# Kernel optimization log

Measured on AMD Instinct MI355X. Metric: run time of the kernel, lower is better.

## Reference

```python
import jax, jax.numpy as jnp
import numpy as np
from jax import lax

DN = ('NCHW', 'OIHW', 'NCHW')
BETA = 0.25


def _conv(x, w, b, stride, pad):
    y = lax.conv_general_dilated(x, w, (stride, stride), [(pad, pad), (pad, pad)],
                                 dimension_numbers=DN)
    return y + b[None, :, None, None]


def _convT(x, w, b, stride, pad, opad):
    # torch ConvTranspose2d(w: [in,out,kh,kw]) == dilated conv with flipped, transposed kernel
    k = w.shape[2]
    wf = jnp.transpose(w, (1, 0, 2, 3))[:, :, ::-1, ::-1]
    lo = k - 1 - pad
    hi = k - 1 - pad + opad
    y = lax.conv_general_dilated(x, wf, (1, 1), [(lo, hi), (lo, hi)],
                                 lhs_dilation=(stride, stride), dimension_numbers=DN)
    return y + b[None, :, None, None]


def setup_inputs() -> dict:
    key = jax.random.key(0)
    ks = jax.random.split(key, 16)
    s = 0.05
    inp = {
        'x': jax.random.normal(ks[0], (64, 3, 125, 125), jnp.float32),
        'enc_w1': jax.random.normal(ks[1], (32, 3, 3, 3), jnp.float32) * s,
        'enc_b1': jnp.zeros((32,), jnp.float32),
        'enc_w2': jax.random.normal(ks[2], (64, 32, 3, 3), jnp.float32) * s,
        'enc_b2': jnp.zeros((64,), jnp.float32),
        'enc_w3': jax.random.normal(ks[3], (64, 64, 1, 1), jnp.float32) * s,
        'enc_b3': jnp.zeros((64,), jnp.float32),
        'codebook': jax.random.normal(ks[4], (512, 64), jnp.float32),
        'dec_w1': jax.random.normal(ks[5], (64, 64, 3, 3), jnp.float32) * s,  # torch [in,out,kh,kw]
        'dec_b1': jnp.zeros((64,), jnp.float32),
        'dec_w2': jax.random.normal(ks[6], (64, 32, 3, 3), jnp.float32) * s,
        'dec_b2': jnp.zeros((32,), jnp.float32),
        'dec_w3': jax.random.normal(ks[7], (32, 3, 2, 2), jnp.float32) * s,
        'dec_b3': jnp.zeros((3,), jnp.float32),
    }
    return inp


def reference(x, enc_w1, enc_b1, enc_w2, enc_b2, enc_w3, enc_b3, codebook,
              dec_w1, dec_b1, dec_w2, dec_b2, dec_w3, dec_b3):
    # Encoder
    z = jax.nn.relu(_conv(x, enc_w1, enc_b1, 2, 1))
    z = jax.nn.relu(_conv(z, enc_w2, enc_b2, 2, 1))
    z = _conv(z, enc_w3, enc_b3, 1, 0)  # [B, D, h, w]

    # VQ (training mode)
    zp = jnp.transpose(z, (0, 2, 3, 1))  # [B, h, w, D]
    flat = zp.reshape(-1, zp.shape[-1])  # [N, D]
    d = (jnp.sum(flat * flat, axis=1, keepdims=True)
         + jnp.sum(codebook * codebook, axis=1)
         - 2.0 * flat @ codebook.T)  # [N, K]
    idx = jnp.argmin(d, axis=1)
    q = codebook[idx].reshape(zp.shape)

    q_latent_loss = jnp.mean((q - lax.stop_gradient(zp)) ** 2)
    e_latent_loss = jnp.mean((zp - lax.stop_gradient(q)) ** 2)
    e_q_loss = q_latent_loss + BETA * e_latent_loss

    q_st = zp + lax.stop_gradient(q - zp)  # straight-through
    e = jnp.transpose(q_st, (0, 3, 1, 2))

    # Decoder
    h = jax.nn.relu(_convT(e, dec_w1, dec_b1, 2, 1, 1))
    h = jax.nn.relu(_convT(h, dec_w2, dec_b2, 2, 1, 1))
    x_recon = _convT(h, dec_w3, dec_b3, 1, 2, 0)

    recon_loss = jnp.sum((x_recon - x) ** 2)
    loss_sum = e_q_loss + recon_loss
    return (loss_sum, e_q_loss, recon_loss, x_recon)
```

## Files before the change

kernel.cpp:

```cpp
#include <hip/hip_runtime.h>

#define DEV __device__ __forceinline__
typedef unsigned short u16;
typedef __bf16 bf16x8 __attribute__((ext_vector_type(8)));
typedef float f32x4 __attribute__((ext_vector_type(4)));

DEV u16 f2bf(float f) {
  unsigned u = __float_as_uint(f);
  u += 0x7FFF + ((u >> 16) & 1);
  return (u16)(u >> 16);
}


__global__ __launch_bounds__(256) void k_prep(
    const float* __restrict__ ew1, const float* __restrict__ ew2,
    const float* __restrict__ ew3, const float* __restrict__ dw1,
    const float* __restrict__ dw2, const float* __restrict__ dw3,
    const float* __restrict__ cb,
    float* __restrict__ wc1p, float* __restrict__ wc3p,
    u16* __restrict__ w3f, float* __restrict__ c2,
    u16* __restrict__ w2f, u16* __restrict__ wt1f, u16* __restrict__ wt2f,
    u16* __restrict__ cbf,
    const float* __restrict__ x, float* __restrict__ xp) {
  if (blockIdx.x >= 582) {
    int idx = (blockIdx.x - 582) * 256 + threadIdx.x;
    int c4 = idx & 31;
    int r  = (idx >> 5) % 129;
    int cbp = (idx >> 5) / 129;
    int ih = r - 1;
    float4 v = make_float4(0.f, 0.f, 0.f, 0.f);
    if ((unsigned)ih < 125u) {
      const float* rp = x + (cbp * 125 + ih) * 125;
      int iw0 = c4 * 4 - 1;
      if (iw0 >= 0)        v.x = rp[iw0];
      if (iw0 + 1 < 125)   v.y = rp[iw0 + 1];
      if (iw0 + 2 < 125)   v.z = rp[iw0 + 2];
      if (iw0 + 3 < 125)   v.w = rp[iw0 + 3];
    }
    *(float4*)(xp + (cbp * 129 + r) * 128 + c4 * 4) = v;
    return;
  }
  int i = blockIdx.x * 256 + threadIdx.x;
  if (i < 864) {
    int cl = i & 7; int t = i >> 3; int tap = t % 9; t /= 9; int ci = t % 3; int cog = t / 3;
    wc1p[i] = ew1[((cog * 8 + cl) * 3 + ci) * 9 + tap];
  } else if (i < 4960) {
    int j = i - 864; int cl = j & 7; int t = j >> 3; int ci = t & 63; int cog = t >> 6;
    wc3p[j] = ew3[(cog * 8 + cl) * 64 + ci];
  } else if (i < 9056) {
    int j = i - 4960;
    int jj = j & 7; int lane = (j >> 3) & 63; int tp = (j >> 9) & 3; int hl = j >> 11;
    int kh = tp >> 1, kw = tp & 1;
    int ci = ((lane >> 4) << 3) + jj; int co = lane & 15;
    float wv = (co < 3) ? dw3[((ci * 3 + co) * 2 + kh) * 2 + kw] : 0.f;
    u16 hi = f2bf(wv);
    if (hl == 0) w3f[j] = hi;
    else         w3f[j] = f2bf(wv - __uint_as_float((unsigned)hi << 16));
  } else if (i < 9568) {
    int k = i - 9056;
    const float4* c4 = (const float4*)(cb + (k << 6));
    float s = 0.f;
    #pragma unroll
    for (int q = 0; q < 16; ++q) { float4 v = c4[q]; s += v.x*v.x + v.y*v.y + v.z*v.z + v.w*v.w; }
    c2[k] = s;
  } else if (i < 28000) {
    int j = i - 9568;
    int jj = j & 7; int lane = (j >> 3) & 63; int nf = (j >> 9) & 3; int kt = j >> 11;
    int kh = kt / 3, kw = kt % 3;
    int ci = ((lane >> 4) << 3) + jj; int co = (nf << 4) + (lane & 15);
    w2f[j] = f2bf(ew2[((co * 32 + ci) * 3 + kh) * 3 + kw]);
  } else if (i < 64864) {
    int j = i - 28000;
    int jj = j & 7; int lane = (j >> 3) & 63; int nf = (j >> 9) & 3; int s = (j >> 11) & 1; int kt = j >> 12;
    int kh = kt / 3, kw = kt % 3;
    int ci = (s << 5) + ((lane >> 4) << 3) + jj; int co = (nf << 4) + (lane & 15);
    wt1f[j] = f2bf(dw1[((ci * 64 + co) * 3 + kh) * 3 + kw]);
  } else if (i < 83296) {
    int j = i - 64864;
    int jj = j & 7; int lane = (j >> 3) & 63; int nf = (j >> 9) & 1; int s = (j >> 10) & 1; int kt = j >> 11;
    int kh = kt / 3, kw = kt % 3;
    int ci = (s << 5) + ((lane >> 4) << 3) + jj; int co = (nf << 4) + (lane & 15);
    wt2f[j] = f2bf(dw2[((ci * 32 + co) * 3 + kh) * 3 + kw]);
  } else if (i < 148832) {
    int j = i - 83296;
    int jj = j & 7; int lane = (j >> 3) & 63; int nt = (j >> 9) & 31; int ks = (j >> 14) & 1; int hl = j >> 15;
    int ci = (ks << 5) + ((lane >> 4) << 3) + jj;
    int code = (nt << 4) + (lane & 15);
    float v = cb[(code << 6) + ci];
    u16 hi = f2bf(v);
    cbf[j] = hl ? f2bf(v - __uint_as_float((unsigned)hi << 16)) : hi;
  }
}

__global__ __launch_bounds__(256) void k_conv1(
    const float* __restrict__ xp, const float* __restrict__ wp,
    const float* __restrict__ bias, u16* __restrict__ z1t) {
  __shared__ u16 st[256 * 34];
  int t = threadIdx.x;
  int slab = blockIdx.x & 15, b = blockIdx.x >> 4;
  int tx = t & 15, ty = (t >> 4) & 3, cg = t >> 6;
  int oh = slab * 4 + ty;
  int co0 = cg * 8;
  const float* wcg = wp + cg * 216;
  float acc[8][4];
  #pragma unroll
  for (int c = 0; c < 8; ++c) {
    float bv = bias[co0 + c];
    #pragma unroll
    for (int s = 0; s < 4; ++s) acc[c][s] = bv;
  }
  #pragma unroll
  for (int ci = 0; ci < 3; ++ci) {
    #pragma unroll
    for (int kh = 0; kh < 3; ++kh) {
      const float* rp = xp + ((b * 3 + ci) * 129 + (2 * oh + kh)) * 128 + 8 * tx;
      float4 qa = *(const float4*)rp;
      float4 qb = *(const float4*)(rp + 4);
      float v8 = rp[8];
      float v[9] = {qa.x, qa.y, qa.z, qa.w, qb.x, qb.y, qb.z, qb.w, v8};
      #pragma unroll
      for (int kw = 0; kw < 3; ++kw) {
        const float* wq = wcg + (ci * 9 + kh * 3 + kw) * 8;
        float4 wa = *(const float4*)wq;
        float4 wb = *(const float4*)(wq + 4);
        float w8[8] = {wa.x, wa.y, wa.z, wa.w, wb.x, wb.y, wb.z, wb.w};
        #pragma unroll
        for (int s = 0; s < 4; ++s) {
          float in = v[2 * s + kw];
          #pragma unroll
          for (int c = 0; c < 8; ++c) acc[c][s] = fmaf(in, w8[c], acc[c][s]);
        }
      }
    }
  }
  #pragma unroll
  for (int s = 0; s < 4; ++s) {
    bool wok = (tx * 4 + s) < 63;
    unsigned p0 = 0, p1 = 0, p2 = 0, p3 = 0;
    if (wok) {
      p0 = f2bf(fmaxf(acc[0][s], 0.f)) | ((unsigned)f2bf(fmaxf(acc[1][s], 0.f)) << 16);
      p1 = f2bf(fmaxf(acc[2][s], 0.f)) | ((unsigned)f2bf(fmaxf(acc[3][s], 0.f)) << 16);
      p2 = f2bf(fmaxf(acc[4][s], 0.f)) | ((unsigned)f2bf(fmaxf(acc[5][s], 0.f)) << 16);
      p3 = f2bf(fmaxf(acc[6][s], 0.f)) | ((unsigned)f2bf(fmaxf(acc[7][s], 0.f)) << 16);
    }
    int lpix = tx * 16 + ty * 4 + s;
    *(uint4*)&st[lpix * 34 + co0] = make_uint4(p0, p1, p2, p3);
  }
  __syncthreads();
  {
    int p = t;
    int ow = (p >> 4) * 4 + (p & 3);
    int ohl = (p >> 2) & 3;
    int oho = slab * 4 + ohl;
    if (oho < 63) {
      const u16* lp = &st[p * 34];
      uint4 a0 = *(const uint4*)(lp);
      uint4 a1 = *(const uint4*)(lp + 8);
      uint4 a2 = *(const uint4*)(lp + 16);
      uint4 a3 = *(const uint4*)(lp + 24);
      uint4* gp = (uint4*)(z1t + ((b * 63 + oho) * 64 + ow) * 32);
      gp[0] = a0; gp[1] = a1; gp[2] = a2; gp[3] = a3;
    }
  }
}

__global__ __launch_bounds__(256) void k_conv2(
    const u16* __restrict__ z1t, const u16* __restrict__ wf,
    const float* __restrict__ bias, float* __restrict__ z2) {
  int t = threadIdx.x;
  int lane = t & 63, wv = t >> 6;
  int n = lane & 15, q = lane >> 4;
  int raw = blockIdx.x;
  int wg = ((raw & 7) << 8) + (raw >> 3);
  int oh = wg & 31, b = wg >> 5;
  int xt = wv & 1, ch = wv >> 1;
  int xA = xt * 16 + n;
  f32x4 acc[2] = {{0,0,0,0},{0,0,0,0}};
  #pragma unroll
  for (int kh = 0; kh < 3; ++kh) {
    int ih = 2 * oh - 1 + kh;
    bool yok = (unsigned)ih < 63u;
    #pragma unroll
    for (int kw = 0; kw < 3; ++kw) {
      int iw = 2 * xA - 1 + kw;
      bool ok = yok && (iw >= 0);
      bf16x8 a = {};
      if (ok) a = *(const bf16x8*)(z1t + ((b * 63 + ih) * 64 + iw) * 32 + q * 8);
      int kt = kh * 3 + kw;
      const u16* wb = wf + ((kt << 2) + (ch << 1)) * 512 + lane * 8;
      bf16x8 b0 = *(const bf16x8*)wb;
      bf16x8 b1 = *(const bf16x8*)(wb + 512);
      acc[0] = __builtin_amdgcn_mfma_f32_16x16x32_bf16(a, b0, acc[0], 0, 0, 0);
      acc[1] = __builtin_amdgcn_mfma_f32_16x16x32_bf16(a, b1, acc[1], 0, 0, 0);
    }
  }
  #pragma unroll
  for (int j = 0; j < 2; ++j) {
    int co = ((ch << 1) + j) * 16 + n;
    float bv = bias[co];
    float4 rv = make_float4(fmaxf(acc[j][0] + bv, 0.f), fmaxf(acc[j][1] + bv, 0.f),
                            fmaxf(acc[j][2] + bv, 0.f), fmaxf(acc[j][3] + bv, 0.f));
    *(float4*)(z2 + ((b * 64 + co) * 32 + oh) * 32 + xt * 16 + q * 4) = rv;
  }
}

__global__ __launch_bounds__(256) void k_conv3(
    const float* __restrict__ in, const float* __restrict__ wp,
    const float* __restrict__ bias, float* __restrict__ z3,
    u16* __restrict__ z3h, u16* __restrict__ z3l) {
  __shared__ u16 lh[128 * 72];
  __shared__ u16 ll[128 * 72];
  int t = threadIdx.x;
  int pxg = blockIdx.x & 7; int b = blockIdx.x >> 3;
  int pxi = t & 31, cog = t >> 5;
  int px0 = pxg * 128 + pxi * 4;
  const float* wcg = wp + cog * 512;
  int co0 = cog * 8;
  float acc[8][4];
  #pragma unroll
  for (int c = 0; c < 8; ++c) {
    float bv = bias[co0 + c];
    #pragma unroll
    for (int s = 0; s < 4; ++s) acc[c][s] = bv;
  }
  const float* ip = in + (b << 16) + px0;
  for (int ci = 0; ci < 64; ++ci) {
    float4 v = *(const float4*)(ip + (ci << 10));
    float4 wa = *(const float4*)(wcg + ci * 8);
    float4 wb = *(const float4*)(wcg + ci * 8 + 4);
    float w8[8] = {wa.x, wa.y, wa.z, wa.w, wb.x, wb.y, wb.z, wb.w};
    #pragma unroll
    for (int c = 0; c < 8; ++c) {
      acc[c][0] = fmaf(v.x, w8[c], acc[c][0]);
      acc[c][1] = fmaf(v.y, w8[c], acc[c][1]);
      acc[c][2] = fmaf(v.z, w8[c], acc[c][2]);
      acc[c][3] = fmaf(v.w, w8[c], acc[c][3]);
    }
  }
  float* op = z3 + ((b << 6) + co0) * 1024 + px0;
  #pragma unroll
  for (int c = 0; c < 8; ++c)
    *(float4*)(op + (c << 10)) = make_float4(acc[c][0], acc[c][1], acc[c][2], acc[c][3]);
  #pragma unroll
  for (int s = 0; s < 4; ++s) {
    unsigned h[4], l[4];
    #pragma unroll
    for (int g = 0; g < 4; ++g) {
      float v0 = acc[2 * g][s], v1 = acc[2 * g + 1][s];
      u16 h0 = f2bf(v0), h1 = f2bf(v1);
      u16 l0 = f2bf(v0 - __uint_as_float((unsigned)h0 << 16));
      u16 l1 = f2bf(v1 - __uint_as_float((unsigned)h1 << 16));
      h[g] = h0 | ((unsigned)h1 << 16);
      l[g] = l0 | ((unsigned)l1 << 16);
    }
    int la = (pxi * 4 + s) * 72 + co0;
    *(uint4*)&lh[la] = make_uint4(h[0], h[1], h[2], h[3]);
    *(uint4*)&ll[la] = make_uint4(l[0], l[1], l[2], l[3]);
  }
  __syncthreads();
  {
    int p = t >> 1, half = t & 1;
    int la = p * 72 + half * 32;
    uint4 h0 = *(uint4*)&lh[la],      h1 = *(uint4*)&lh[la + 8];
    uint4 h2 = *(uint4*)&lh[la + 16], h3 = *(uint4*)&lh[la + 24];
    uint4 l0 = *(uint4*)&ll[la],      l1 = *(uint4*)&ll[la + 8];
    uint4 l2 = *(uint4*)&ll[la + 16], l3 = *(uint4*)&ll[la + 24];
    long gp = ((long)b * 1024 + pxg * 128 + p) * 64 + half * 32;
    uint4* oh = (uint4*)(z3h + gp);
    uint4* ol = (uint4*)(z3l + gp);
    oh[0] = h0; oh[1] = h1; oh[2] = h2; oh[3] = h3;
    ol[0] = l0; ol[1] = l1; ol[2] = l2; ol[3] = l3;
  }
}

__global__ __launch_bounds__(256) void k_vqpf(
    const u16* __restrict__ z3h, const u16* __restrict__ z3l,
    const u16* __restrict__ cbf, const float* __restrict__ c2v,
    const float* __restrict__ z3, const float* __restrict__ cb,
    u16* __restrict__ et, float* __restrict__ acc) {
  int t = threadIdx.x;
  int lane = t & 63, wv = t >> 6;
  int n = lane & 15, q = lane >> 4;
  int p0 = blockIdx.x * 64;
  bf16x8 Ah[4][2], Al[4][2];
  #pragma unroll
  for (int mt = 0; mt < 4; ++mt) {
    const u16* ap = z3h + (p0 + mt * 16 + n) * 64 + q * 8;
    const u16* al = z3l + (p0 + mt * 16 + n) * 64 + q * 8;
    Ah[mt][0] = *(const bf16x8*)ap;  Ah[mt][1] = *(const bf16x8*)(ap + 32);
    Al[mt][0] = *(const bf16x8*)al;  Al[mt][1] = *(const bf16x8*)(al + 32);
  }
  float bs[4][4]; int bix[4][4];
  #pragma unroll
  for (int mt = 0; mt < 4; ++mt)
    #pragma unroll
    for (int r = 0; r < 4; ++r) { bs[mt][r] = 3.4e38f; bix[mt][r] = 0; }
  for (int nt0 = 0; nt0 < 8; ++nt0) {
    int nt = wv * 8 + nt0;
    const u16* bp = cbf + lane * 8;
    bf16x8 Bh0 = *(const bf16x8*)(bp + (nt << 9));
    bf16x8 Bh1 = *(const bf16x8*)(bp + ((32 + nt) << 9));
    bf16x8 Bl0 = *(const bf16x8*)(bp + ((64 + nt) << 9));
    bf16x8 Bl1 = *(const bf16x8*)(bp + ((96 + nt) << 9));
    float c2 = c2v[(nt << 4) + n];
    #pragma unroll
    for (int mt = 0; mt < 4; ++mt) {
      f32x4 a = {0.f, 0.f, 0.f, 0.f};
      a = __builtin_amdgcn_mfma_f32_16x16x32_bf16(Ah[mt][0], Bh0, a, 0, 0, 0);
      a = __builtin_amdgcn_mfma_f32_16x16x32_bf16(Ah[mt][1], Bh1, a, 0, 0, 0);
      a = __builtin_amdgcn_mfma_f32_16x16x32_bf16(Al[mt][0], Bh0, a, 0, 0, 0);
      a = __builtin_amdgcn_mfma_f32_16x16x32_bf16(Al[mt][1], Bh1, a, 0, 0, 0);
      a = __builtin_amdgcn_mfma_f32_16x16x32_bf16(Ah[mt][0], Bl0, a, 0, 0, 0);
      a = __builtin_amdgcn_mfma_f32_16x16x32_bf16(Ah[mt][1], Bl1, a, 0, 0, 0);
      int idx = (nt << 4) + n;
      #pragma unroll
      for (int r = 0; r < 4; ++r) {
        float sc = fmaf(-2.f, a[r], c2);
        if (sc < bs[mt][r]) { bs[mt][r] = sc; bix[mt][r] = idx; }
      }
    }
  }
  #pragma unroll
  for (int off = 8; off > 0; off >>= 1) {
    #pragma unroll
    for (int mt = 0; mt < 4; ++mt)
      #pragma unroll
      for (int r = 0; r < 4; ++r) {
        float os = __shfl_xor(bs[mt][r], off, 16);
        int oi = __shfl_xor(bix[mt][r], off, 16);
        if (os < bs[mt][r] || (os == bs[mt][r] && oi < bix[mt][r])) {
          bs[mt][r] = os; bix[mt][r] = oi;
        }
      }
  }
  __shared__ float ls[4][64];
  __shared__ int   li[4][64];
  __shared__ int   lfin[64];
  if (n == 0) {
    #pragma unroll
    for (int mt = 0; mt < 4; ++mt)
      #pragma unroll
      for (int r = 0; r < 4; ++r) {
        int px = mt * 16 + q * 4 + r;
        ls[wv][px] = bs[mt][r];
        li[wv][px] = bix[mt][r];
      }
  }
  __syncthreads();
  if (t < 64) {
    float best = ls[0][t]; int bi = li[0][t];
    #pragma unroll
    for (int w = 1; w < 4; ++w) {
      float s = ls[w][t]; int ii = li[w][t];
      if (s < best || (s == best && ii < bi)) { best = s; bi = ii; }
    }
    lfin[t] = bi;
  }
  __syncthreads();
  int pxl = t >> 2, ciq = t & 3;
  int ng = p0 + pxl;
  int bb = ng >> 10, hw = ng & 1023;
  int bi = lfin[pxl];
  const float* zp = z3 + (bb << 16) + hw;
  const float4* cq = (const float4*)(cb + (bi << 6) + (ciq << 4));
  float lsum = 0.f;
  unsigned pk[8];
  #pragma unroll
  for (int i = 0; i < 4; ++i) {
    float4 c = cq[i];
    int cbase = (ciq << 4) + (i << 2);
    float zv, df;
    zv = zp[(cbase + 0) << 10]; df = c.x - zv; lsum = fmaf(df, df, lsum);
    zv = zp[(cbase + 1) << 10]; df = c.y - zv; lsum = fmaf(df, df, lsum);
    zv = zp[(cbase + 2) << 10]; df = c.z - zv; lsum = fmaf(df, df, lsum);
    zv = zp[(cbase + 3) << 10]; df = c.w - zv; lsum = fmaf(df, df, lsum);
    pk[2 * i]     = f2bf(c.x) | ((unsigned)f2bf(c.y) << 16);
    pk[2 * i + 1] = f2bf(c.z) | ((unsigned)f2bf(c.w) << 16);
  }
  uint4* ep = (uint4*)(et + ((long)ng << 6) + (ciq << 4));
  ep[0] = make_uint4(pk[0], pk[1], pk[2], pk[3]);
  ep[1] = make_uint4(pk[4], pk[5], pk[6], pk[7]);
  __shared__ float red[256];
  red[t] = lsum; __syncthreads();
  #pragma unroll
  for (int s = 128; s > 0; s >>= 1) {
    if (t < s) red[t] += red[t + s];
    __syncthreads();
  }
  if (t == 0) atomicAdd(acc + 0, red[0]);
}

__global__ __launch_bounds__(256) void k_convT1(
    const u16* __restrict__ et, const u16* __restrict__ wf,
    const float* __restrict__ bias, u16* __restrict__ h1t) {
  __shared__ u16 wl[36 * 512];
  __shared__ u16 st[4][64 * 34];
  int t = threadIdx.x;
  int lane = t & 63, wv = t >> 6;
  int yw = wv & 1, xt = wv >> 1;
  int raw = blockIdx.x;
  int wg = ((raw & 7) << 7) + (raw >> 3);
  int cog = wg & 1;
  int yg = (wg >> 1) & 7;
  int b = wg >> 4;
  {
    const uint4* gw = (const uint4*)wf;
    uint4* lw = (uint4*)wl;
    #pragma unroll
    for (int k = 0; k < 9; ++k) {
      int i = t + 256 * k;
      int slot = i >> 6, within = i & 63;
      int kt = slot >> 2, j = (slot >> 1) & 1, ks = slot & 1;
      int goff = (kt << 12) + (((ks << 2) + (cog << 1) + j) << 9);
      lw[i] = gw[(goff >> 3) + within];
    }
  }
  int n = lane & 15, q = lane >> 4;
  int m = xt * 16 + n;
  __syncthreads();
  for (int iter = 0; iter < 2; ++iter) {
    int y = yg * 4 + iter * 2 + yw;
    const u16* base0 = et + (((b * 32 + y) * 32) << 6) + q * 8;
    bf16x8 P00a, P00b, P01a = {}, P01b = {}, P10a = {}, P10b = {}, P11a = {}, P11b = {};
    { const u16* p = base0 + (m << 6); P00a = *(const bf16x8*)p; P00b = *(const bf16x8*)(p + 32); }
    if (m + 1 < 32) { const u16* p = base0 + ((m + 1) << 6); P01a = *(const bf16x8*)p; P01b = *(const bf16x8*)(p + 32); }
    if (y + 1 < 32) {
      const u16* base1 = base0 + (32 << 6);
      { const u16* p = base1 + (m << 6); P10a = *(const bf16x8*)p; P10b = *(const bf16x8*)(p + 32); }
      if (m + 1 < 32) { const u16* p = base1 + ((m + 1) << 6); P11a = *(const bf16x8*)p; P11b = *(const bf16x8*)(p + 32); }
    }
    f32x4 accE[2][2] = {};
    f32x4 accO[2][2] = {};
    #pragma unroll
    for (int kw = 0; kw < 3; ++kw) {
      int pwi = (kw == 1) ? 0 : 1;
      bf16x8 A0a = (kw == 0) ? P01a : P00a;
      bf16x8 A0b = (kw == 0) ? P01b : P00b;
      bf16x8 A1a = (kw == 0) ? P11a : P10a;
      bf16x8 A1b = (kw == 0) ? P11b : P10b;
      #pragma unroll
      for (int j = 0; j < 2; ++j) {
        const u16* wE  = wl + ((((3 + kw) << 2) + (j << 1)) << 9) + lane * 8;
        const u16* wO0 = wl + (((kw << 2) + (j << 1)) << 9) + lane * 8;
        const u16* wO2 = wl + ((((6 + kw) << 2) + (j << 1)) << 9) + lane * 8;
        bf16x8 bE0 = *(const bf16x8*)wE;
        bf16x8 bE1 = *(const bf16x8*)(wE + 512);
        accE[j][pwi] = __builtin_amdgcn_mfma_f32_16x16x32_bf16(A0a, bE0, accE[j][pwi], 0, 0, 0);
        accE[j][pwi] = __builtin_amdgcn_mfma_f32_16x16x32_bf16(A0b, bE1, accE[j][pwi], 0, 0, 0);
        bf16x8 bO00 = *(const bf16x8*)wO0;
        bf16x8 bO01 = *(const bf16x8*)(wO0 + 512);
        accO[j][pwi] = __builtin_amdgcn_mfma_f32_16x16x32_bf16(A1a, bO00, accO[j][pwi], 0, 0, 0);
        accO[j][pwi] = __builtin_amdgcn_mfma_f32_16x16x32_bf16(A1b, bO01, accO[j][pwi], 0, 0, 0);
        bf16x8 bO20 = *(const bf16x8*)wO2;
        bf16x8 bO21 = *(const bf16x8*)(wO2 + 512);
        accO[j][pwi] = __builtin_amdgcn_mfma_f32_16x16x32_bf16(A0a, bO20, accO[j][pwi], 0, 0, 0);
        accO[j][pwi] = __builtin_amdgcn_mfma_f32_16x16x32_bf16(A0b, bO21, accO[j][pwi], 0, 0, 0);
      }
    }
    #pragma unroll
    for (int j = 0; j < 2; ++j) {
      int col = j * 16 + n;
      float bv = bias[cog * 32 + col];
      #pragma unroll
      for (int pw = 0; pw < 2; ++pw)
        #pragma unroll
        for (int r = 0; r < 4; ++r) {
          int ow = 2 * (xt * 16 + q * 4 + r) + pw;
          st[yw * 2 + 0][ow * 34 + col] = f2bf(fmaxf(accE[j][pw][r] + bv, 0.f));
          st[yw * 2 + 1][ow * 34 + col] = f2bf(fmaxf(accO[j][pw][r] + bv, 0.f));
        }
    }
    __syncthreads();
    {
      int row = t >> 6, ow = t & 63;
      const u16* lp = &st[row][ow * 34];
      uint4* gp = (uint4*)(h1t + (((b * 64 + yg * 8 + iter * 4 + row) * 64 + ow) << 6) + cog * 32);
      gp[0] = *(const uint4*)(lp);
      gp[1] = *(const uint4*)(lp + 8);
      gp[2] = *(const uint4*)(lp + 16);
      gp[3] = *(const uint4*)(lp + 24);
    }
    __syncthreads();
  }
}

__global__ __launch_bounds__(256) void k_convT2(
    const u16* __restrict__ h1t, const u16* __restrict__ wf,
    const float* __restrict__ bias, u16* __restrict__ h2t) {
  __shared__ u16 wl[18432];
  __shared__ u16 st[2][128 * 34];
  int t = threadIdx.x;
  int lane = t & 63, xt = t >> 6;
  int n = lane & 15, q = lane >> 4;
  int raw = blockIdx.x;
  int wg = ((raw & 7) << 7) + (raw >> 3);
  int yg = wg & 15, b = wg >> 4;
  {
    const uint4* gw = (const uint4*)wf;
    uint4* lw = (uint4*)wl;
    #pragma unroll
    for (int k = 0; k < 9; ++k) lw[t + 256 * k] = gw[t + 256 * k];
  }
  int m = xt * 16 + n;
  __syncthreads();
  for (int yp = 0; yp < 4; ++yp) {
    int y = yg * 4 + yp;
    const u16* base0 = h1t + (((b * 64 + y) * 64) << 6) + q * 8;
    bf16x8 P00a, P00b, P01a = {}, P01b = {}, P10a = {}, P10b = {}, P11a = {}, P11b = {};
    { const u16* p = base0 + (m << 6); P00a = *(const bf16x8*)p; P00b = *(const bf16x8*)(p + 32); }
    if (m + 1 < 64) { const u16* p = base0 + ((m + 1) << 6); P01a = *(const bf16x8*)p; P01b = *(const bf16x8*)(p + 32); }
    if (y + 1 < 64) {
      const u16* base1 = base0 + (64 << 6);
      { const u16* p = base1 + (m << 6); P10a = *(const bf16x8*)p; P10b = *(const bf16x8*)(p + 32); }
      if (m + 1 < 64) { const u16* p = base1 + ((m + 1) << 6); P11a = *(const bf16x8*)p; P11b = *(const bf16x8*)(p + 32); }
    }
    f32x4 accE[2][2] = {};
    f32x4 accO[2][2] = {};
    #pragma unroll
    for (int kw = 0; kw < 3; ++kw) {
      int pwi = (kw == 1) ? 0 : 1;
      bf16x8 A0a = (kw == 0) ? P01a : P00a;
      bf16x8 A0b = (kw == 0) ? P01b : P00b;
      bf16x8 A1a = (kw == 0) ? P11a : P10a;
      bf16x8 A1b = (kw == 0) ? P11b : P10b;
      const u16* wbE = wl + ((3 + kw) << 11) + lane * 8;
      const u16* wbO0 = wl + (kw << 11) + lane * 8;
      const u16* wbO2 = wl + ((6 + kw) << 11) + lane * 8;
      #pragma unroll
      for (int nf = 0; nf < 2; ++nf) {
        bf16x8 bE0 = *(const bf16x8*)(wbE + nf * 512);
        bf16x8 bE1 = *(const bf16x8*)(wbE + (2 + nf) * 512);
        accE[nf][pwi] = __builtin_amdgcn_mfma_f32_16x16x32_bf16(A0a, bE0, accE[nf][pwi], 0, 0, 0);
        accE[nf][pwi] = __builtin_amdgcn_mfma_f32_16x16x32_bf16(A0b, bE1, accE[nf][pwi], 0, 0, 0);
        bf16x8 bO00 = *(const bf16x8*)(wbO0 + nf * 512);
        bf16x8 bO01 = *(const bf16x8*)(wbO0 + (2 + nf) * 512);
        accO[nf][pwi] = __builtin_amdgcn_mfma_f32_16x16x32_bf16(A1a, bO00, accO[nf][pwi], 0, 0, 0);
        accO[nf][pwi] = __builtin_amdgcn_mfma_f32_16x16x32_bf16(A1b, bO01, accO[nf][pwi], 0, 0, 0);
        bf16x8 bO20 = *(const bf16x8*)(wbO2 + nf * 512);
        bf16x8 bO21 = *(const bf16x8*)(wbO2 + (2 + nf) * 512);
        accO[nf][pwi] = __builtin_amdgcn_mfma_f32_16x16x32_bf16(A0a, bO20, accO[nf][pwi], 0, 0, 0);
        accO[nf][pwi] = __builtin_amdgcn_mfma_f32_16x16x32_bf16(A0b, bO21, accO[nf][pwi], 0, 0, 0);
      }
    }
    #pragma unroll
    for (int nf = 0; nf < 2; ++nf) {
      int co = nf * 16 + n;
      float bv = bias[co];
      #pragma unroll
      for (int pw = 0; pw < 2; ++pw)
        #pragma unroll
        for (int r = 0; r < 4; ++r) {
          int ow = 2 * (xt * 16 + q * 4 + r) + pw;
          st[0][ow * 34 + co] = f2bf(fmaxf(accE[nf][pw][r] + bv, 0.f));
          st[1][ow * 34 + co] = f2bf(fmaxf(accO[nf][pw][r] + bv, 0.f));
        }
    }
    __syncthreads();
    {
      int ow = t >> 1, sg = t & 1;
      #pragma unroll
      for (int l = 0; l < 2; ++l) {
        const u16* lp = &st[l][ow * 34 + sg * 16];
        unsigned w0 = *(const unsigned*)(lp + 0), w1 = *(const unsigned*)(lp + 2);
        unsigned w2 = *(const unsigned*)(lp + 4), w3 = *(const unsigned*)(lp + 6);
        unsigned w4 = *(const unsigned*)(lp + 8), w5 = *(const unsigned*)(lp + 10);
        unsigned w6 = *(const unsigned*)(lp + 12), w7 = *(const unsigned*)(lp + 14);
        uint4* gp = (uint4*)(h2t + ((((b * 128 + yg * 8 + yp * 2 + l) * 128) + ow) << 5) + sg * 16);
        gp[0] = make_uint4(w0, w1, w2, w3);
        gp[1] = make_uint4(w4, w5, w6, w7);
      }
    }
    __syncthreads();
  }
}

__global__ __launch_bounds__(256) void k_convT3(
    const u16* __restrict__ h2t, const u16* __restrict__ w3f,
    const float* __restrict__ bias, const float* __restrict__ x,
    float* __restrict__ xr, float* __restrict__ psum) {
  int t = threadIdx.x;
  int lane = t & 63, wv = t >> 6;
  int n = lane & 15, q = lane >> 4;
  int raw = blockIdx.x;
  int wg = ((raw & 7) << 8) + (raw >> 3);
  int rg = wg & 31, b = wg >> 5;
  int oh0 = rg * 4;
  const u16* wbp = w3f + lane * 8;
  bf16x8 Bh0 = *(const bf16x8*)(wbp);
  bf16x8 Bh1 = *(const bf16x8*)(wbp + 512);
  bf16x8 Bh2 = *(const bf16x8*)(wbp + 1024);
  bf16x8 Bh3 = *(const bf16x8*)(wbp + 1536);
  bf16x8 Bl0 = *(const bf16x8*)(wbp + 2048);
  bf16x8 Bl1 = *(const bf16x8*)(wbp + 2560);
  bf16x8 Bl2 = *(const bf16x8*)(wbp + 3072);
  bf16x8 Bl3 = *(const bf16x8*)(wbp + 3584);
  float bv = (n < 3) ? bias[n] : 0.f;
  float lsum = 0.f;
  if (oh0 <= 121) {
    const u16* rbase = h2t + (((long)b * 128 + (oh0 + 1)) << 12) + q * 8;
    #pragma unroll
    for (int ti = 0; ti < 2; ++ti) {
      int tt = wv + ti * 4;
      int c1 = tt * 16 + n + 1;
      int c2 = c1 + 1;
      bf16x8 A[5][2];
      #pragma unroll
      for (int j = 0; j < 5; ++j) {
        A[j][0] = (bf16x8){}; A[j][1] = (bf16x8){};
        const u16* rp = rbase + ((long)j << 12);
        if (c1 < 128) A[j][0] = *(const bf16x8*)(rp + (c1 << 5));
        if (c2 < 128) A[j][1] = *(const bf16x8*)(rp + (c2 << 5));
      }
      f32x4 ac[4] = {};
      #pragma unroll
      for (int k = 0; k < 4; ++k) {
        ac[k] = __builtin_amdgcn_mfma_f32_16x16x32_bf16(A[k][0],     Bh3, ac[k], 0, 0, 0);
        ac[k] = __builtin_amdgcn_mfma_f32_16x16x32_bf16(A[k][1],     Bh2, ac[k], 0, 0, 0);
        ac[k] = __builtin_amdgcn_mfma_f32_16x16x32_bf16(A[k + 1][0], Bh1, ac[k], 0, 0, 0);
        ac[k] = __builtin_amdgcn_mfma_f32_16x16x32_bf16(A[k + 1][1], Bh0, ac[k], 0, 0, 0);
        ac[k] = __builtin_amdgcn_mfma_f32_16x16x32_bf16(A[k][0],     Bl3, ac[k], 0, 0, 0);
        ac[k] = __builtin_amdgcn_mfma_f32_16x16x32_bf16(A[k][1],     Bl2, ac[k], 0, 0, 0);
        ac[k] = __builtin_amdgcn_mfma_f32_16x16x32_bf16(A[k + 1][0], Bl1, ac[k], 0, 0, 0);
        ac[k] = __builtin_amdgcn_mfma_f32_16x16x32_bf16(A[k + 1][1], Bl0, ac[k], 0, 0, 0);
      }
      if (n < 3) {
        int ow0 = tt * 16 + q * 4;
        #pragma unroll
        for (int k = 0; k < 4; ++k) {
          int oh = oh0 + k;
          int o = b * 46875 + n * 15625 + oh * 125 + ow0;
          if (ow0 + 3 < 125) {
            float4 v = make_float4(ac[k][0] + bv, ac[k][1] + bv, ac[k][2] + bv, ac[k][3] + bv);
            float4 xv = *(const float4*)(x + o);
            *(float4*)(xr + o) = v;
            float d0 = v.x - xv.x, d1 = v.y - xv.y, d2 = v.z - xv.z, d3 = v.w - xv.w;
            lsum += d0 * d0 + d1 * d1 + d2 * d2 + d3 * d3;
          } else {
            #pragma unroll
            for (int r = 0; r < 4; ++r) {
              if (ow0 + r < 125) {
                float v = ac[k][r] + bv;
                xr[o + r] = v;
                float d = v - x[o + r];
                lsum = fmaf(d, d, lsum);
              }
            }
          }
        }
      }
    }
  } else {
    int oh = 124;
    const u16* row1 = h2t + (((long)b * 128 + (oh + 1)) << 12) + q * 8;
    const u16* row2 = row1 + 4096;
    #pragma unroll
    for (int ti = 0; ti < 2; ++ti) {
      int tt = wv + ti * 4;
      int c1 = tt * 16 + n + 1;
      int c2 = c1 + 1;
      bf16x8 a11 = {}, a12 = {}, a21 = {}, a22 = {};
      if (c1 < 128) { a11 = *(const bf16x8*)(row1 + (c1 << 5));
                      a21 = *(const bf16x8*)(row2 + (c1 << 5)); }
      if (c2 < 128) { a12 = *(const bf16x8*)(row1 + (c2 << 5));
                      a22 = *(const bf16x8*)(row2 + (c2 << 5)); }
      f32x4 a = {0.f, 0.f, 0.f, 0.f};
      a = __builtin_amdgcn_mfma_f32_16x16x32_bf16(a11, Bh3, a, 0, 0, 0);
      a = __builtin_amdgcn_mfma_f32_16x16x32_bf16(a12, Bh2, a, 0, 0, 0);
      a = __builtin_amdgcn_mfma_f32_16x16x32_bf16(a21, Bh1, a, 0, 0, 0);
      a = __builtin_amdgcn_mfma_f32_16x16x32_bf16(a22, Bh0, a, 0, 0, 0);
      a = __builtin_amdgcn_mfma_f32_16x16x32_bf16(a11, Bl3, a, 0, 0, 0);
      a = __builtin_amdgcn_mfma_f32_16x16x32_bf16(a12, Bl2, a, 0, 0, 0);
      a = __builtin_amdgcn_mfma_f32_16x16x32_bf16(a21, Bl1, a, 0, 0, 0);
      a = __builtin_amdgcn_mfma_f32_16x16x32_bf16(a22, Bl0, a, 0, 0, 0);
      if (n < 3) {
        int ow0 = tt * 16 + q * 4;
        int o = b * 46875 + n * 15625 + oh * 125 + ow0;
        if (ow0 + 3 < 125) {
          float4 v = make_float4(a[0] + bv, a[1] + bv, a[2] + bv, a[3] + bv);
          float4 xv = *(const float4*)(x + o);
          *(float4*)(xr + o) = v;
          float d0 = v.x - xv.x, d1 = v.y - xv.y, d2 = v.z - xv.z, d3 = v.w - xv.w;
          lsum += d0 * d0 + d1 * d1 + d2 * d2 + d3 * d3;
        } else {
          #pragma unroll
          for (int r = 0; r < 4; ++r) {
            if (ow0 + r < 125) {
              float v = a[r] + bv;
              xr[o + r] = v;
              float d = v - x[o + r];
              lsum = fmaf(d, d, lsum);
            }
          }
        }
      }
    }
  }
  __shared__ float red[256];
  red[t] = lsum; __syncthreads();
  #pragma unroll
  for (int s = 128; s > 0; s >>= 1) {
    if (t < s) red[t] += red[t + s];
    __syncthreads();
  }
  if (t == 0) psum[raw] = red[0];
}

__global__ __launch_bounds__(256) void k_fin(
    const float* __restrict__ acc, const float* __restrict__ psum,
    float* __restrict__ out) {
  int t = threadIdx.x;
  float s = 0.f;
  for (int i = t; i < 2048; i += 256) s += psum[i];
  __shared__ float red[256];
  red[t] = s; __syncthreads();
  #pragma unroll
  for (int k = 128; k > 0; k >>= 1) {
    if (t < k) red[t] += red[t + k];
    __syncthreads();
  }
  if (t == 0) {
    float eq  = 1.25f * acc[0] / 4194304.0f;
    float rec = red[0];
    out[0] = eq + rec;
    out[1] = eq;
    out[2] = rec;
  }
}

extern "C" void kernel_launch(void* const* d_in, const int* in_sizes, int n_in,
                              void* d_out, int out_size, void* d_ws, size_t ws_size,
                              hipStream_t stream) {
  (void)in_sizes; (void)n_in; (void)out_size; (void)ws_size;
  const float* x   = (const float*)d_in[0];
  const float* ew1 = (const float*)d_in[1];
  const float* eb1 = (const float*)d_in[2];
  const float* ew2 = (const float*)d_in[3];
  const float* eb2 = (const float*)d_in[4];
  const float* ew3 = (const float*)d_in[5];
  const float* eb3 = (const float*)d_in[6];
  const float* cb  = (const float*)d_in[7];
  const float* dw1 = (const float*)d_in[8];
  const float* db1 = (const float*)d_in[9];
  const float* dw2 = (const float*)d_in[10];
  const float* db2 = (const float*)d_in[11];
  const float* dw3 = (const float*)d_in[12];
  const float* db3 = (const float*)d_in[13];
  float* out = (float*)d_out;
  char*  ws  = (char*)d_ws;

  float*  acc  = (float*)(ws + 0);
  float*  c2   = (float*)(ws + 256);
  float*  wc1p = (float*)(ws + 4096);
  float*  wc3p = (float*)(ws + 8192);
  u16*    w3f  = (u16*)  (ws + 24576);
  u16*    w2f  = (u16*)  (ws + 36864);
  u16*    wt1f = (u16*)  (ws + 73728);
  u16*    wt2f = (u16*)  (ws + 147456);
  float*  psum = (float*)(ws + 184320);
  u16*    cbf  = (u16*)  (ws + 262144);
  u16*    z1t  = (u16*)  (ws + 1048576);
  float*  z2   = (float*)(ws + 18874368);
  float*  z3   = (float*)(ws + 35651584);
  u16*    et   = (u16*)  (ws + 54525952);
  u16*    h1t  = (u16*)  (ws + 1048576);
  u16*    h2t  = (u16*)  (ws + 67108864);
  u16*    z3h  = (u16*)  (ws + 134217728);
  u16*    z3l  = (u16*)  (ws + 142606336);
  float*  xp   = (float*)(ws + 150994944);

  hipMemsetAsync(acc, 0, 64, stream);
  k_prep  <<<3678, 256, 0, stream>>>(ew1, ew2, ew3, dw1, dw2, dw3, cb,
                                     wc1p, wc3p, w3f, c2, w2f, wt1f, wt2f, cbf,
                                     x, xp);
  k_conv1 <<<1024, 256, 0, stream>>>(xp, wc1p, eb1, z1t);
  k_conv2 <<<2048, 256, 0, stream>>>(z1t, w2f, eb2, z2);
  k_conv3 <<<512,  256, 0, stream>>>(z2, wc3p, eb3, z3, z3h, z3l);
  k_vqpf  <<<1024, 256, 0, stream>>>(z3h, z3l, cbf, c2, z3, cb, et, acc);
  k_convT1<<<1024, 256, 0, stream>>>(et, wt1f, db1, h1t);
  k_convT2<<<1024, 256, 0, stream>>>(h1t, wt2f, db2, h2t);
  k_convT3<<<2048, 256, 0, stream>>>(h2t, w3f, db3, x, out + 3, psum);
  k_fin   <<<1,    256, 0, stream>>>(acc, psum, out);
}
```

Before: 283.6 us.

## Run 1x1 conv3 on MFMA with split-bf16 operands and NHWC z2 layout

conv2 now writes its ReLU output as hi/lo bf16 pairs in pixel-major (NHWC) layout through a shared-memory transpose, instead of fp32 NCHW. conv3, the 1x1 conv, becomes a bf16 MFMA GEMM using the three-term split-precision product (hh, lh, hl) to approximate fp32, with weights pre-packed in prep. This replaces scalar FMA loops and reduces conv2's store traffic. The cost is extra MFMA work per output, an added LDS round trip in conv2, and a small precision change from dropping the lo*lo term.

```diff
diff --git a/kernel.cpp b/kernel.cpp
--- a/kernel.cpp
+++ b/kernel.cpp
@@ -17,13 +17,13 @@
     const float* __restrict__ ew3, const float* __restrict__ dw1,
     const float* __restrict__ dw2, const float* __restrict__ dw3,
     const float* __restrict__ cb,
-    float* __restrict__ wc1p, float* __restrict__ wc3p,
+    float* __restrict__ wc1p, u16* __restrict__ wc3b,
     u16* __restrict__ w3f, float* __restrict__ c2,
     u16* __restrict__ w2f, u16* __restrict__ wt1f, u16* __restrict__ wt2f,
     u16* __restrict__ cbf,
     const float* __restrict__ x, float* __restrict__ xp) {
-  if (blockIdx.x >= 582) {
-    int idx = (blockIdx.x - 582) * 256 + threadIdx.x;
+  if (blockIdx.x >= 598) {
+    int idx = (blockIdx.x - 598) * 256 + threadIdx.x;
     int c4 = idx & 31;
     int r  = (idx >> 5) % 129;
     int cbp = (idx >> 5) / 129;
@@ -44,11 +44,16 @@
   if (i < 864) {
     int cl = i & 7; int t = i >> 3; int tap = t % 9; t /= 9; int ci = t % 3; int cog = t / 3;
     wc1p[i] = ew1[((cog * 8 + cl) * 3 + ci) * 9 + tap];
-  } else if (i < 4960) {
-    int j = i - 864; int cl = j & 7; int t = j >> 3; int ci = t & 63; int cog = t >> 6;
-    wc3p[j] = ew3[(cog * 8 + cl) * 64 + ci];
   } else if (i < 9056) {
-    int j = i - 4960;
+    int j = i - 864;
+    int jj = j & 7; int lane = (j >> 3) & 63; int nf = (j >> 9) & 3; int ks = (j >> 11) & 1; int hl = j >> 12;
+    int co = (nf << 4) + (lane & 15);
+    int ci = (ks << 5) + ((lane >> 4) << 3) + jj;
+    float v = ew3[co * 64 + ci];
+    u16 hi = f2bf(v);
+    wc3b[j] = hl ? f2bf(v - __uint_as_float((unsigned)hi << 16)) : hi;
+  } else if (i < 13152) {
+    int j = i - 9056;
     int jj = j & 7; int lane = (j >> 3) & 63; int tp = (j >> 9) & 3; int hl = j >> 11;
     int kh = tp >> 1, kw = tp & 1;
     int ci = ((lane >> 4) << 3) + jj; int co = lane & 15;
@@ -56,33 +61,33 @@
     u16 hi = f2bf(wv);
     if (hl == 0) w3f[j] = hi;
     else         w3f[j] = f2bf(wv - __uint_as_float((unsigned)hi << 16));
-  } else if (i < 9568) {
-    int k = i - 9056;
+  } else if (i < 13664) {
+    int k = i - 13152;
     const float4* c4 = (const float4*)(cb + (k << 6));
     float s = 0.f;
     #pragma unroll
     for (int q = 0; q < 16; ++q) { float4 v = c4[q]; s += v.x*v.x + v.y*v.y + v.z*v.z + v.w*v.w; }
     c2[k] = s;
-  } else if (i < 28000) {
-    int j = i - 9568;
+  } else if (i < 32096) {
+    int j = i - 13664;
     int jj = j & 7; int lane = (j >> 3) & 63; int nf = (j >> 9) & 3; int kt = j >> 11;
     int kh = kt / 3, kw = kt % 3;
     int ci = ((lane >> 4) << 3) + jj; int co = (nf << 4) + (lane & 15);
     w2f[j] = f2bf(ew2[((co * 32 + ci) * 3 + kh) * 3 + kw]);
-  } else if (i < 64864) {
-    int j = i - 28000;
+  } else if (i < 68960) {
+    int j = i - 32096;
     int jj = j & 7; int lane = (j >> 3) & 63; int nf = (j >> 9) & 3; int s = (j >> 11) & 1; int kt = j >> 12;
     int kh = kt / 3, kw = kt % 3;
     int ci = (s << 5) + ((lane >> 4) << 3) + jj; int co = (nf << 4) + (lane & 15);
     wt1f[j] = f2bf(dw1[((ci * 64 + co) * 3 + kh) * 3 + kw]);
-  } else if (i < 83296) {
-    int j = i - 64864;
+  } else if (i < 87392) {
+    int j = i - 68960;
     int jj = j & 7; int lane = (j >> 3) & 63; int nf = (j >> 9) & 1; int s = (j >> 10) & 1; int kt = j >> 11;
     int kh = kt / 3, kw = kt % 3;
     int ci = (s << 5) + ((lane >> 4) << 3) + jj; int co = (nf << 4) + (lane & 15);
     wt2f[j] = f2bf(dw2[((ci * 32 + co) * 3 + kh) * 3 + kw]);
-  } else if (i < 148832) {
-    int j = i - 83296;
+  } else if (i < 152928) {
+    int j = i - 87392;
     int jj = j & 7; int lane = (j >> 3) & 63; int nt = (j >> 9) & 31; int ks = (j >> 14) & 1; int hl = j >> 15;
     int ci = (ks << 5) + ((lane >> 4) << 3) + jj;
     int code = (nt << 4) + (lane & 15);
@@ -166,7 +171,9 @@
 
 __global__ __launch_bounds__(256) void k_conv2(
     const u16* __restrict__ z1t, const u16* __restrict__ wf,
-    const float* __restrict__ bias, float* __restrict__ z2) {
+    const float* __restrict__ bias, u16* __restrict__ z2h, u16* __restrict__ z2l) {
+  __shared__ u16 sh[32 * 72];
+  __shared__ u16 sl[32 * 72];
   int t = threadIdx.x;
   int lane = t & 63, wv = t >> 6;
   int n = lane & 15, q = lane >> 4;
@@ -198,64 +205,86 @@
   for (int j = 0; j < 2; ++j) {
     int co = ((ch << 1) + j) * 16 + n;
     float bv = bias[co];
-    float4 rv = make_float4(fmaxf(acc[j][0] + bv, 0.f), fmaxf(acc[j][1] + bv, 0.f),
-                            fmaxf(acc[j][2] + bv, 0.f), fmaxf(acc[j][3] + bv, 0.f));
-    *(float4*)(z2 + ((b * 64 + co) * 32 + oh) * 32 + xt * 16 + q * 4) = rv;
+    #pragma unroll
+    for (int r = 0; r < 4; ++r) {
+      int ow = xt * 16 + q * 4 + r;
+      float v = fmaxf(acc[j][r] + bv, 0.f);
+      u16 h = f2bf(v);
+      u16 l = f2bf(v - __uint_as_float((unsigned)h << 16));
+      sh[ow * 72 + co] = h;
+      sl[ow * 72 + co] = l;
+    }
+  }
+  __syncthreads();
+  {
+    int ow = t >> 3, sg = t & 7;
+    uint4 hv = *(const uint4*)&sh[ow * 72 + sg * 8];
+    uint4 lv = *(const uint4*)&sl[ow * 72 + sg * 8];
+    long gp = ((long)(b * 1024 + oh * 32 + ow) << 6) + sg * 8;
+    *(uint4*)(z2h + gp) = hv;
+    *(uint4*)(z2l + gp) = lv;
   }
 }
 
 __global__ __launch_bounds__(256) void k_conv3(
-    const float* __restrict__ in, const float* __restrict__ wp,
-    const float* __restrict__ bias, float* __restrict__ z3,
-    u16* __restrict__ z3h, u16* __restrict__ z3l) {
+    const u16* __restrict__ z2h, const u16* __restrict__ z2l,
+    const u16* __restrict__ wcb, const float* __restrict__ bias,
+    float* __restrict__ z3, u16* __restrict__ z3h, u16* __restrict__ z3l) {
   __shared__ u16 lh[128 * 72];
   __shared__ u16 ll[128 * 72];
   int t = threadIdx.x;
+  int lane = t & 63, wv = t >> 6;
+  int n = lane & 15, q = lane >> 4;
   int pxg = blockIdx.x & 7; int b = blockIdx.x >> 3;
-  int pxi = t & 31, cog = t >> 5;
-  int px0 = pxg * 128 + pxi * 4;
-  const float* wcg = wp + cog * 512;
-  int co0 = cog * 8;
-  float acc[8][4];
-  #pragma unroll
-  for (int c = 0; c < 8; ++c) {
-    float bv = bias[co0 + c];
-    #pragma unroll
-    for (int s = 0; s < 4; ++s) acc[c][s] = bv;
-  }
-  const float* ip = in + (b << 16) + px0;
-  for (int ci = 0; ci < 64; ++ci) {
-    float4 v = *(const float4*)(ip + (ci << 10));
-    float4 wa = *(const float4*)(wcg + ci * 8);
-    float4 wb = *(const float4*)(wcg + ci * 8 + 4);
-    float w8[8] = {wa.x, wa.y, wa.z, wa.w, wb.x, wb.y, wb.z, wb.w};
-    #pragma unroll
-    for (int c = 0; c < 8; ++c) {
-      acc[c][0] = fmaf(v.x, w8[c], acc[c][0]);
-      acc[c][1] = fmaf(v.y, w8[c], acc[c][1]);
-      acc[c][2] = fmaf(v.z, w8[c], acc[c][2]);
-      acc[c][3] = fmaf(v.w, w8[c], acc[c][3]);
-    }
-  }
-  float* op = z3 + ((b << 6) + co0) * 1024 + px0;
-  #pragma unroll
-  for (int c = 0; c < 8; ++c)
-    *(float4*)(op + (c << 10)) = make_float4(acc[c][0], acc[c][1], acc[c][2], acc[c][3]);
-  #pragma unroll
-  for (int s = 0; s < 4; ++s) {
-    unsigned h[4], l[4];
-    #pragma unroll
-    for (int g = 0; g < 4; ++g) {
-      float v0 = acc[2 * g][s], v1 = acc[2 * g + 1][s];
-      u16 h0 = f2bf(v0), h1 = f2bf(v1);
-      u16 l0 = f2bf(v0 - __uint_as_float((unsigned)h0 << 16));
-      u16 l1 = f2bf(v1 - __uint_as_float((unsigned)h1 << 16));
-      h[g] = h0 | ((unsigned)h1 << 16);
-      l[g] = l0 | ((unsigned)l1 << 16);
-    }
-    int la = (pxi * 4 + s) * 72 + co0;
-    *(uint4*)&lh[la] = make_uint4(h[0], h[1], h[2], h[3]);
-    *(uint4*)&ll[la] = make_uint4(l[0], l[1], l[2], l[3]);
+  bf16x8 Ah[2][2], Al[2][2];
+  #pragma unroll
+  for (int mti = 0; mti < 2; ++mti) {
+    int px = b * 1024 + pxg * 128 + (wv * 2 + mti) * 16 + n;
+    const u16* ap = z2h + px * 64 + q * 8;
+    const u16* al = z2l + px * 64 + q * 8;
+    Ah[mti][0] = *(const bf16x8*)ap;  Ah[mti][1] = *(const bf16x8*)(ap + 32);
+    Al[mti][0] = *(const bf16x8*)al;  Al[mti][1] = *(const bf16x8*)(al + 32);
+  }
+  f32x4 acc[2][4];
+  #pragma unroll
+  for (int nf = 0; nf < 4; ++nf) {
+    const u16* wb = wcb + (nf << 9) + lane * 8;
+    bf16x8 Bh0 = *(const bf16x8*)wb;
+    bf16x8 Bh1 = *(const bf16x8*)(wb + 2048);
+    bf16x8 Bl0 = *(const bf16x8*)(wb + 4096);
+    bf16x8 Bl1 = *(const bf16x8*)(wb + 6144);
+    #pragma unroll
+    for (int mti = 0; mti < 2; ++mti) {
+      f32x4 a = {0.f, 0.f, 0.f, 0.f};
+      a = __builtin_amdgcn_mfma_f32_16x16x32_bf16(Ah[mti][0], Bh0, a, 0, 0, 0);
+      a = __builtin_amdgcn_mfma_f32_16x16x32_bf16(Ah[mti][1], Bh1, a, 0, 0, 0);
+      a = __builtin_amdgcn_mfma_f32_16x16x32_bf16(Al[mti][0], Bh0, a, 0, 0, 0);
+      a = __builtin_amdgcn_mfma_f32_16x16x32_bf16(Al[mti][1], Bh1, a, 0, 0, 0);
+      a = __builtin_amdgcn_mfma_f32_16x16x32_bf16(Ah[mti][0], Bl0, a, 0, 0, 0);
+      a = __builtin_amdgcn_mfma_f32_16x16x32_bf16(Ah[mti][1], Bl1, a, 0, 0, 0);
+      acc[mti][nf] = a;
+    }
+  }
+  #pragma unroll
+  for (int mti = 0; mti < 2; ++mti) {
+    int pxl0 = (wv * 2 + mti) * 16 + q * 4;
+    #pragma unroll
+    for (int nf = 0; nf < 4; ++nf) {
+      int co = (nf << 4) + n;
+      float bv = bias[co];
+      float v[4];
+      #pragma unroll
+      for (int r = 0; r < 4; ++r) v[r] = acc[mti][nf][r] + bv;
+      *(float4*)(z3 + (((b << 6) + co) << 10) + pxg * 128 + pxl0) =
+          make_float4(v[0], v[1], v[2], v[3]);
+      #pragma unroll
+      for (int r = 0; r < 4; ++r) {
+        u16 h = f2bf(v[r]);
+        u16 l = f2bf(v[r] - __uint_as_float((unsigned)h << 16));
+        lh[(pxl0 + r) * 72 + co] = h;
+        ll[(pxl0 + r) * 72 + co] = l;
+      }
+    }
   }
   __syncthreads();
   {
@@ -751,7 +780,7 @@
   float*  acc  = (float*)(ws + 0);
   float*  c2   = (float*)(ws + 256);
   float*  wc1p = (float*)(ws + 4096);
-  float*  wc3p = (float*)(ws + 8192);
+  u16*    wc3b = (u16*)  (ws + 8192);
   u16*    w3f  = (u16*)  (ws + 24576);
   u16*    w2f  = (u16*)  (ws + 36864);
   u16*    wt1f = (u16*)  (ws + 73728);
@@ -759,7 +788,8 @@
   float*  psum = (float*)(ws + 184320);
   u16*    cbf  = (u16*)  (ws + 262144);
   u16*    z1t  = (u16*)  (ws + 1048576);
-  float*  z2   = (float*)(ws + 18874368);
+  u16*    z2h  = (u16*)  (ws + 18874368);
+  u16*    z2l  = (u16*)  (ws + 27262976);
   float*  z3   = (float*)(ws + 35651584);
   u16*    et   = (u16*)  (ws + 54525952);
   u16*    h1t  = (u16*)  (ws + 1048576);
@@ -769,12 +799,12 @@
   float*  xp   = (float*)(ws + 150994944);
 
   hipMemsetAsync(acc, 0, 64, stream);
-  k_prep  <<<3678, 256, 0, stream>>>(ew1, ew2, ew3, dw1, dw2, dw3, cb,
-                                     wc1p, wc3p, w3f, c2, w2f, wt1f, wt2f, cbf,
+  k_prep  <<<3694, 256, 0, stream>>>(ew1, ew2, ew3, dw1, dw2, dw3, cb,
+                                     wc1p, wc3b, w3f, c2, w2f, wt1f, wt2f, cbf,
                                      x, xp);
   k_conv1 <<<1024, 256, 0, stream>>>(xp, wc1p, eb1, z1t);
-  k_conv2 <<<2048, 256, 0, stream>>>(z1t, w2f, eb2, z2);
-  k_conv3 <<<512,  256, 0, stream>>>(z2, wc3p, eb3, z3, z3h, z3l);
+  k_conv2 <<<2048, 256, 0, stream>>>(z1t, w2f, eb2, z2h, z2l);
+  k_conv3 <<<512,  256, 0, stream>>>(z2h, z2l, wc3b, eb3, z3, z3h, z3l);
   k_vqpf  <<<1024, 256, 0, stream>>>(z3h, z3l, cbf, c2, z3, cb, et, acc);
   k_convT1<<<1024, 256, 0, stream>>>(et, wt1f, db1, h1t);
   k_convT2<<<1024, 256, 0, stream>>>(h1t, wt2f, db2, h2t);
```

After: 275.1 us. 1.03x faster.
